# Optimization experiments

Hardware: AMD Instinct MI355X
Metric: run time of the kernel (lower is better)

The kernel has to match this reference:

```python
import jax, jax.numpy as jnp
import numpy as np

B, T, S, H, V, L = 64, 60, 60, 512, 32000, 2
NEG = -1.0e9  # matches torch mask value -1000000000.0


def setup_inputs() -> dict:
    key = jax.random.key(0)
    ks = jax.random.split(key, 12)
    sc = 0.05
    return {
        "indices": jax.random.randint(ks[0], (B, T), 0, V),
        "enc_output": jax.random.normal(ks[1], (B, S, H), dtype=jnp.float32),
        "de_lens": jax.random.randint(ks[2], (B,), 1, S + 1),
        "emb": jax.random.normal(ks[3], (V, H), dtype=jnp.float32) * sc,
        "w_ih": jax.random.normal(ks[4], (L, 4 * H, H), dtype=jnp.float32) * sc,
        "w_hh": jax.random.normal(ks[5], (L, 4 * H, H), dtype=jnp.float32) * sc,
        "b_ih": jnp.zeros((L, 4 * H), dtype=jnp.float32),
        "b_hh": jnp.zeros((L, 4 * H), dtype=jnp.float32),
        "lin_w": jax.random.normal(ks[6], (L, H, 2 * H), dtype=jnp.float32) * sc,
        "lin_b": jnp.zeros((L, H), dtype=jnp.float32),
        "out_w": jax.random.normal(ks[7], (V, H), dtype=jnp.float32) * sc,
        "out_b": jnp.zeros((V,), dtype=jnp.float32),
    }


def _lstm_seq(x, w_ih, w_hh, b_ih, b_hh):
    # x: [B,T,H] -> hidden states [B,T,H]; torch gate order i,f,g,o
    xg = jnp.einsum('bth,gh->btg', x, w_ih) + b_ih  # [B,T,4H]
    h0 = jnp.zeros((x.shape[0], w_hh.shape[1]), x.dtype)

    def step(carry, xg_t):
        h, c = carry
        g = xg_t + h @ w_hh.T + b_hh
        i, f, gg, o = jnp.split(g, 4, axis=-1)
        c = jax.nn.sigmoid(f) * c + jax.nn.sigmoid(i) * jnp.tanh(gg)
        h = jax.nn.sigmoid(o) * jnp.tanh(c)
        return (h, c), h

    _, hs = jax.lax.scan(step, (h0, h0), jnp.swapaxes(xg, 0, 1))
    return jnp.swapaxes(hs, 0, 1)


def reference(indices, enc_output, de_lens, emb, w_ih, w_hh, b_ih, b_hh,
              lin_w, lin_b, out_w, out_b):
    # additive length mask over encoder positions: [B,S]
    mask = jnp.where(jnp.arange(S)[None, :] < de_lens[:, None], 0.0, NEG).astype(enc_output.dtype)
    x = emb[indices]  # [B,T,H]
    for l in range(L):
        dec = _lstm_seq(x, w_ih[l], w_hh[l], b_ih[l], b_hh[l])  # [B,T,H]
        scores = jnp.einsum('bth,bsh->bts', dec, enc_output) + mask[:, None, :]
        probs = jax.nn.softmax(scores, axis=-1)
        attn = jnp.einsum('bts,bsh->bth', probs, enc_output)
        cat = jnp.concatenate([dec, attn], axis=-1)  # [B,T,2H]
        x = jnp.einsum('btk,hk->bth', cat, lin_w[l]) + lin_b[l]
    return jnp.einsum('bth,vh->btv', x, out_w) + out_b  # [B,T,V]
```

## Files before the change

kernel.cpp:

```cpp
#include <hip/hip_runtime.h>
#include <hip/hip_bf16.h>
#include <math.h>

#define B_ 64
#define T_ 60
#define S_ 60
#define H_ 512
#define V_ 32000
#define L_ 2
#define BT_ (B_*T_)
#define LDSROW 40
#define LDSROW2 72

typedef __attribute__((ext_vector_type(8))) short short8;
typedef __attribute__((ext_vector_type(4))) float f32x4;
typedef __attribute__((ext_vector_type(4))) unsigned int u32x4;

__device__ __forceinline__ short f2bf(float x) {
  __hip_bfloat16 h = __float2bfloat16(x);
  return __builtin_bit_cast(short, h);
}
__device__ __forceinline__ float bf2f(short s) {
  unsigned int u = ((unsigned int)(unsigned short)s) << 16;
  return __builtin_bit_cast(float, u);
}
__device__ __forceinline__ float sigm(float x) { return 1.f / (1.f + __expf(-x)); }
__device__ __forceinline__ float tanh_(float x) {
  float e = __expf(-2.f * fabsf(x));
  float t = (1.f - e) / (1.f + e);
  return x >= 0.f ? t : -t;
}

__device__ __forceinline__ void ld4g(const char* p, u32x4* q, bool llc) {
  if (llc)
    asm volatile("global_load_dwordx4 %0, %4, off sc0 sc1\n\t"
                 "global_load_dwordx4 %1, %4, off offset:16 sc0 sc1\n\t"
                 "global_load_dwordx4 %2, %4, off offset:32 sc0 sc1\n\t"
                 "global_load_dwordx4 %3, %4, off offset:48 sc0 sc1"
                 : "=v"(q[0]), "=v"(q[1]), "=v"(q[2]), "=v"(q[3]) : "v"(p));
  else
    asm volatile("global_load_dwordx4 %0, %4, off sc0\n\t"
                 "global_load_dwordx4 %1, %4, off offset:16 sc0\n\t"
                 "global_load_dwordx4 %2, %4, off offset:32 sc0\n\t"
                 "global_load_dwordx4 %3, %4, off offset:48 sc0"
                 : "=v"(q[0]), "=v"(q[1]), "=v"(q[2]), "=v"(q[3]) : "v"(p));
}

#define LDSBAR() do { \
    asm volatile("s_waitcnt lgkmcnt(0)" ::: "memory"); \
    __builtin_amdgcn_s_barrier(); \
    __builtin_amdgcn_sched_barrier(0); \
  } while (0)

__global__ __launch_bounds__(256) void convbf_k(const float* __restrict__ src,
                                                short* __restrict__ dst) {
  int g = blockIdx.x * 256 + threadIdx.x;
  const float* s = src + (size_t)g * 8;
  float4 v0 = *(const float4*)s, v1 = *(const float4*)(s + 4);
  short8 o;
  o[0]=f2bf(v0.x); o[1]=f2bf(v0.y); o[2]=f2bf(v0.z); o[3]=f2bf(v0.w);
  o[4]=f2bf(v1.x); o[5]=f2bf(v1.y); o[6]=f2bf(v1.z); o[7]=f2bf(v1.w);
  *(short8*)(dst + (size_t)g * 8) = o;
}

__global__ __launch_bounds__(256) void pack_whh_k(const float* __restrict__ whh,
                                                  short* __restrict__ pk) {
  int idx = blockIdx.x * 256 + threadIdx.x;
  int l = idx >> 17, rem = idx & 131071;
  int n = rem >> 6, k8 = rem & 63;
  int g = n >> 9, j = n & 511;
  int np = (j >> 4) * 64 + g * 16 + (j & 15);
  const float* src = whh + ((size_t)l * 2048 + n) * 512 + k8 * 8;
  float4 v0 = *(const float4*)src, v1 = *(const float4*)(src + 4);
  short8 o;
  o[0]=f2bf(v0.x); o[1]=f2bf(v0.y); o[2]=f2bf(v0.z); o[3]=f2bf(v0.w);
  o[4]=f2bf(v1.x); o[5]=f2bf(v1.y); o[6]=f2bf(v1.z); o[7]=f2bf(v1.w);
  size_t dst = (size_t)l * (2048 * 512) + ((size_t)((np >> 4) * 64 + k8)) * 128 + (np & 15) * 8;
  *(short8*)(pk + dst) = o;
}

__global__ __launch_bounds__(256) void embed_k(const int* __restrict__ idx,
                                               const float* __restrict__ emb,
                                               float* __restrict__ x) {
  int e = blockIdx.x * 256 + threadIdx.x;
  int bt = e >> 9, h = e & (H_ - 1);
  int row = idx[bt];
  x[e] = emb[(size_t)row * H_ + h];
}

template<bool XPOSE>
__global__ __launch_bounds__(256) void gemm_a32_k(
    const float* __restrict__ A, const float* __restrict__ Bw,
    const float* __restrict__ bias1, const float* __restrict__ bias2,
    float* __restrict__ C, short* __restrict__ Cbf, int M, int N, int K) {
  __shared__ short Ahs[128 * LDSROW];
  __shared__ short Als[128 * LDSROW];
  __shared__ short Bs[128 * LDSROW];
  int tid = threadIdx.x;
  int bm = blockIdx.y * 128, bn = blockIdx.x * 128;
  int wid = tid >> 6, lane = tid & 63;
  int wr = wid >> 1, wc = wid & 1;
  int lrow = lane & 15, lk = (lane >> 4) * 8;
  f32x4 acc[4][4];
#pragma unroll
  for (int i = 0; i < 4; ++i)
#pragma unroll
    for (int j = 0; j < 4; ++j) acc[i][j] = (f32x4){0.f, 0.f, 0.f, 0.f};

  int srow = tid >> 2, scol = (tid & 3) * 8;

  for (int k0 = 0; k0 < K; k0 += 32) {
#pragma unroll
    for (int it = 0; it < 2; ++it) {
      int r = srow + it * 64;
      const float* ap = A + (size_t)(bm + r) * K + k0 + scol;
      float4 a0 = *(const float4*)ap, a1 = *(const float4*)(ap + 4);
      float av[8] = {a0.x,a0.y,a0.z,a0.w,a1.x,a1.y,a1.z,a1.w};
      short8 hv, lv;
#pragma unroll
      for (int e = 0; e < 8; ++e) {
        short h = f2bf(av[e]);
        hv[e] = h;
        lv[e] = f2bf(av[e] - bf2f(h));
      }
      *(short8*)(Ahs + r * LDSROW + scol) = hv;
      *(short8*)(Als + r * LDSROW + scol) = lv;
      const float* bp = Bw + (size_t)(bn + r) * K + k0 + scol;
      float4 b0 = *(const float4*)bp, b1 = *(const float4*)(bp + 4);
      short8 bv;
      bv[0]=f2bf(b0.x); bv[1]=f2bf(b0.y); bv[2]=f2bf(b0.z); bv[3]=f2bf(b0.w);
      bv[4]=f2bf(b1.x); bv[5]=f2bf(b1.y); bv[6]=f2bf(b1.z); bv[7]=f2bf(b1.w);
      *(short8*)(Bs + r * LDSROW + scol) = bv;
    }
    __syncthreads();
    short8 ah[4], al[4], bfr[4];
#pragma unroll
    for (int i = 0; i < 4; ++i) {
      ah[i] = *(const short8*)(Ahs + (wr * 64 + i * 16 + lrow) * LDSROW + lk);
      al[i] = *(const short8*)(Als + (wr * 64 + i * 16 + lrow) * LDSROW + lk);
    }
#pragma unroll
    for (int j = 0; j < 4; ++j)
      bfr[j] = *(const short8*)(Bs + (wc * 64 + j * 16 + lrow) * LDSROW + lk);
#pragma unroll
    for (int i = 0; i < 4; ++i)
#pragma unroll
      for (int j = 0; j < 4; ++j) {
        acc[i][j] = __builtin_amdgcn_mfma_f32_16x16x32_bf16(ah[i], bfr[j], acc[i][j], 0, 0, 0);
        acc[i][j] = __builtin_amdgcn_mfma_f32_16x16x32_bf16(al[i], bfr[j], acc[i][j], 0, 0, 0);
      }
    __syncthreads();
  }

#pragma unroll
  for (int j = 0; j < 4; ++j) {
    int col = bn + wc * 64 + j * 16 + lrow;
    float bv = bias1[col] + (bias2 ? bias2[col] : 0.f);
#pragma unroll
    for (int i = 0; i < 4; ++i) {
#pragma unroll
      for (int r = 0; r < 4; ++r) {
        int row = bm + wr * 64 + i * 16 + (lane >> 4) * 4 + r;
        float v = acc[i][j][r] + bv;
        if (XPOSE) {
          int b = row / T_, t = row - b * T_;
          int g = col >> 9, jg = col & 511;
          int c8 = b >> 3, bloc = b & 7, q = jg >> 6;
          int nploc = ((jg >> 4) & 3) * 64 + g * 16 + (jg & 15);
          C[(((size_t)t * 64 + q * 8 + c8) * 8 + bloc) * 256 + nploc] = v;
        } else {
          C[(size_t)row * N + col] = v;
          if (Cbf) Cbf[(size_t)row * N + col] = f2bf(v);
        }
      }
    }
  }
}

__global__ __launch_bounds__(256) void gemm_bb_k(
    const short* __restrict__ A, const short* __restrict__ Bbf,
    const float* __restrict__ bias, float* __restrict__ C) {
  const int N = V_, K = H_;
  int n = blockIdx.x;
  int xcd = n & 7, pos = n >> 3;
  int base = (xcd < 4) ? xcd * 938 : 4 * 938 + (xcd - 4) * 937;
  int wg = base + pos;
  int bm = (wg % 30) * 128;
  int bn = (wg / 30) * 128;

  __shared__ short As[128 * LDSROW2];
  __shared__ short Bs[128 * LDSROW2];
  int tid = threadIdx.x;
  int wid = tid >> 6, lane = tid & 63;
  int wr = wid >> 1, wc = wid & 1;
  int lrow = lane & 15;
  f32x4 acc[4][4];
#pragma unroll
  for (int i = 0; i < 4; ++i)
#pragma unroll
    for (int j = 0; j < 4; ++j) acc[i][j] = (f32x4){0.f, 0.f, 0.f, 0.f};

  int srow = tid >> 2, scol = (tid & 3) * 16;

  for (int k0 = 0; k0 < K; k0 += 64) {
#pragma unroll
    for (int it = 0; it < 2; ++it) {
      int r = srow + it * 64;
      const short* ap = A + (size_t)(bm + r) * K + k0 + scol;
      short8 a0 = *(const short8*)ap, a1 = *(const short8*)(ap + 8);
      *(short8*)(As + r * LDSROW2 + scol) = a0;
      *(short8*)(As + r * LDSROW2 + scol + 8) = a1;
      const short* bp = Bbf + (size_t)(bn + r) * K + k0 + scol;
      short8 b0 = *(const short8*)bp, b1 = *(const short8*)(bp + 8);
      *(short8*)(Bs + r * LDSROW2 + scol) = b0;
      *(short8*)(Bs + r * LDSROW2 + scol + 8) = b1;
    }
    __syncthreads();
#pragma unroll
    for (int kk = 0; kk < 2; ++kk) {
      int lk = kk * 32 + (lane >> 4) * 8;
      short8 af[4], bfr[4];
#pragma unroll
      for (int i = 0; i < 4; ++i)
        af[i] = *(const short8*)(As + (wr * 64 + i * 16 + lrow) * LDSROW2 + lk);
#pragma unroll
      for (int j = 0; j < 4; ++j)
        bfr[j] = *(const short8*)(Bs + (wc * 64 + j * 16 + lrow) * LDSROW2 + lk);
#pragma unroll
      for (int i = 0; i < 4; ++i)
#pragma unroll
        for (int j = 0; j < 4; ++j)
          acc[i][j] = __builtin_amdgcn_mfma_f32_16x16x32_bf16(af[i], bfr[j], acc[i][j], 0, 0, 0);
    }
    __syncthreads();
  }

#pragma unroll
  for (int j = 0; j < 4; ++j) {
    int col = bn + wc * 64 + j * 16 + lrow;
    float bv = bias[col];
#pragma unroll
    for (int i = 0; i < 4; ++i)
#pragma unroll
      for (int r = 0; r < 4; ++r) {
        int row = bm + wr * 64 + i * 16 + (lane >> 4) * 4 + r;
        float v = acc[i][j][r] + bv;
        float* cp = C + (size_t)row * N + col;
        asm volatile("global_store_dword %0, %1, off nt" :: "v"(cp), "v"(v) : "memory");
      }
  }
}

__global__ __launch_bounds__(512, 2) void lstm_seq_k(
    const float* __restrict__ xg,
    const short* __restrict__ whh_pk,
    char* __restrict__ hx,
    float* __restrict__ dec) {
  __shared__ short hhi[16][520];
  __shared__ short hlo[16][520];
  __shared__ float gates[256][20];
  const int tid = threadIdx.x;
  const int bid = blockIdx.x;
  const int c = bid & 7, q = bid >> 3;
  const int w = tid >> 6, lane = tid & 63;
  const int lr = lane & 15, lkg = lane >> 4;

  for (int i = tid; i < 16 * 520; i += 512) {
    ((short*)hhi)[i] = 0;
    ((short*)hlo)[i] = 0;
  }

  short8 wreg[2][16];
#pragma unroll
  for (int nt = 0; nt < 2; ++nt)
#pragma unroll
    for (int kt = 0; kt < 16; ++kt)
      wreg[nt][kt] = *(const short8*)(whh_pk +
          ((size_t)((q * 16 + w * 2 + nt) * 64 + kt * 4 + lkg)) * 128 + lr * 8);

  const bool epi = (tid < 256);
  const int bloc_e = tid & 7;
  const int p_e = (tid >> 3) & 31;
  const int j0 = p_e * 2;
  const int s = tid & 255;
  char* grp = hx + (size_t)c * 65536;

  float cc0 = 0.f, cc1 = 0.f;
  __syncthreads();

  for (int t = 0; t < T_; ++t) {
    const unsigned tgt = (unsigned)t;
    float2 xgv[4];
    const int rw0 = (j0 >> 4) * 64 + (j0 & 15);
    if (epi) {
      const float* xb = xg + ((size_t)t * 64 + bid) * 2048 + bloc_e * 256;
#pragma unroll
      for (int g = 0; g < 4; ++g) xgv[g] = *(const float2*)(xb + rw0 + g * 16);
      asm volatile("" ::: "memory");
    } else {
      const char* base = grp + (size_t)(t & 1) * 32768;
      const char* pA = base + (size_t)s * 64;
      const char* pB = base + (size_t)(s + 256) * 64;
      u32x4 qA[4], qB[4];
      ld4g(pA, qA, false);
      ld4g(pB, qB, false);
      for (unsigned a = 0;; ++a) {
        asm volatile("s_waitcnt vmcnt(0)" ::: "memory");
        __builtin_amdgcn_sched_barrier(0);
        unsigned bad = 0;
#pragma unroll
        for (int i = 0; i < 4; ++i) bad |= (qA[i][2] ^ tgt) | (qB[i][2] ^ tgt);
        if (!bad) break;
        __builtin_amdgcn_s_sleep(1);
        bool llc = (a & 1) != 0;
        ld4g(pA, qA, llc);
        ld4g(pB, qB, llc);
      }
      u32x4 hA = {qA[0][0], qA[1][0], qA[2][0], qA[3][0]};
      u32x4 lA = {qA[0][1], qA[1][1], qA[2][1], qA[3][1]};
      u32x4 hB = {qB[0][0], qB[1][0], qB[2][0], qB[3][0]};
      u32x4 lB = {qB[0][1], qB[1][1], qB[2][1], qB[3][1]};
      *(u32x4*)(&hhi[s >> 6][(s & 63) * 8]) = hA;
      *(u32x4*)(&hlo[s >> 6][(s & 63) * 8]) = lA;
      *(u32x4*)(&hhi[4 + (s >> 6)][(s & 63) * 8]) = hB;
      *(u32x4*)(&hlo[4 + (s >> 6)][(s & 63) * 8]) = lB;
    }
    LDSBAR();

    f32x4 acc[2];
    acc[0] = (f32x4){0.f, 0.f, 0.f, 0.f};
    acc[1] = (f32x4){0.f, 0.f, 0.f, 0.f};
#pragma unroll
    for (int kt = 0; kt < 16; ++kt) {
      short8 ah = *(const short8*)(&hhi[lr][kt * 32 + lkg * 8]);
      short8 al = *(const short8*)(&hlo[lr][kt * 32 + lkg * 8]);
#pragma unroll
      for (int nt = 0; nt < 2; ++nt) {
        acc[nt] = __builtin_amdgcn_mfma_f32_16x16x32_bf16(ah, wreg[nt][kt], acc[nt], 0, 0, 0);
        acc[nt] = __builtin_amdgcn_mfma_f32_16x16x32_bf16(al, wreg[nt][kt], acc[nt], 0, 0, 0);
      }
    }
#pragma unroll
    for (int nt = 0; nt < 2; ++nt)
      *(f32x4*)(&gates[(w * 2 + nt) * 16 + lr][lkg * 4]) = acc[nt];
    LDSBAR();

    if (epi) {
      float gv0[4], gv1[4];
#pragma unroll
      for (int g = 0; g < 4; ++g) {
        int rw = rw0 + g * 16;
        gv0[g] = gates[rw][bloc_e] + xgv[g].x;
        gv1[g] = gates[rw + 1][bloc_e] + xgv[g].y;
      }
      float cn0 = sigm(gv0[1]) * cc0 + sigm(gv0[0]) * tanh_(gv0[2]);
      float hn0 = sigm(gv0[3]) * tanh_(cn0);
      cc0 = cn0;
      float cn1 = sigm(gv1[1]) * cc1 + sigm(gv1[0]) * tanh_(gv1[2]);
      float hn1 = sigm(gv1[3]) * tanh_(cn1);
      cc1 = cn1;
      short hi0 = f2bf(hn0), hi1 = f2bf(hn1);
      short lo0 = f2bf(hn0 - bf2f(hi0)), lo1 = f2bf(hn1 - bf2f(hi1));
      u32x4 hv;
      hv[0] = (unsigned)(unsigned short)hi0 | ((unsigned)(unsigned short)hi1 << 16);
      hv[1] = (unsigned)(unsigned short)lo0 | ((unsigned)(unsigned short)lo1 << 16);
      hv[2] = tgt + 1u;
      hv[3] = tgt + 1u;
      char* pb = grp + (size_t)((t + 1) & 1) * 32768 +
                 ((size_t)(bloc_e * 256 + q * 32 + p_e)) * 16;
      asm volatile("global_store_dwordx4 %0, %1, off sc0" :: "v"(pb), "v"(hv) : "memory");
      asm volatile("global_store_dwordx4 %0, %1, off sc0 sc1" :: "v"(pb), "v"(hv) : "memory");
      float2 dv; dv.x = hn0; dv.y = hn1;
      *(float2*)(dec + ((size_t)(c * 8 + bloc_e) * T_ + t) * H_ + q * 64 + j0) = dv;
    }
    LDSBAR();
  }
}

__global__ __launch_bounds__(256) void attn_k(const float* __restrict__ dec,
                                              const float* __restrict__ enc,
                                              const int* __restrict__ lens,
                                              float* __restrict__ cat) {
  int bt = blockIdx.x;
  int b = bt / T_;
  __shared__ float dsh[H_];
  __shared__ float p[64];
  int tid = threadIdx.x;
  dsh[tid] = dec[(size_t)bt * H_ + tid];
  dsh[tid + 256] = dec[(size_t)bt * H_ + tid + 256];
  __syncthreads();
  int wid = tid >> 6, lane = tid & 63;
  int len = lens[b];
  for (int s = wid; s < S_; s += 4) {
    const float* er = enc + ((size_t)(b * S_ + s)) * H_ + lane * 8;
    float4 e0 = *(const float4*)er, e1 = *(const float4*)(er + 4);
    const float* dr = dsh + lane * 8;
    float sum = e0.x*dr[0] + e0.y*dr[1] + e0.z*dr[2] + e0.w*dr[3]
              + e1.x*dr[4] + e1.y*dr[5] + e1.z*dr[6] + e1.w*dr[7];
#pragma unroll
    for (int off = 32; off > 0; off >>= 1) sum += __shfl_down(sum, off);
    if (lane == 0) p[s] = sum + (s < len ? 0.f : -1.0e9f);
  }
  __syncthreads();
  if (wid == 0) {
    float v = (lane < S_) ? p[lane] : -INFINITY;
    float m = v;
#pragma unroll
    for (int off = 32; off > 0; off >>= 1) m = fmaxf(m, __shfl_down(m, off));
    m = __shfl(m, 0);
    float e = (lane < S_) ? expf(v - m) : 0.f;
    float ssum = e;
#pragma unroll
    for (int off = 32; off > 0; off >>= 1) ssum += __shfl_down(ssum, off);
    ssum = __shfl(ssum, 0);
    if (lane < S_) p[lane] = e / ssum;
  }
  __syncthreads();
  int h = tid * 2;
  float a0 = 0.f, a1 = 0.f;
  for (int s = 0; s < S_; ++s) {
    float ps = p[s];
    const float* er = enc + ((size_t)(b * S_ + s)) * H_ + h;
    a0 += ps * er[0];
    a1 += ps * er[1];
  }
  size_t base = (size_t)bt * (2 * H_);
  cat[base + h]          = dsh[h];
  cat[base + h + 1]      = dsh[h + 1];
  cat[base + H_ + h]     = a0;
  cat[base + H_ + h + 1] = a1;
}

extern "C" void kernel_launch(void* const* d_in, const int* in_sizes, int n_in,
                              void* d_out, int out_size, void* d_ws, size_t ws_size,
                              hipStream_t stream) {
  (void)in_sizes; (void)n_in; (void)out_size; (void)ws_size;
  const int*   indices = (const int*)d_in[0];
  const float* enc     = (const float*)d_in[1];
  const int*   de_lens = (const int*)d_in[2];
  const float* emb     = (const float*)d_in[3];
  const float* w_ih    = (const float*)d_in[4];
  const float* w_hh    = (const float*)d_in[5];
  const float* b_ih    = (const float*)d_in[6];
  const float* b_hh    = (const float*)d_in[7];
  const float* lin_w   = (const float*)d_in[8];
  const float* lin_b   = (const float*)d_in[9];
  const float* out_w   = (const float*)d_in[10];
  const float* out_b   = (const float*)d_in[11];
  float* outp = (float*)d_out;

  char* ws = (char*)d_ws;
  size_t off = 0;
  auto alloc = [&](size_t bytes) -> void* {
    void* p = ws + off; off += (bytes + 255) & ~(size_t)255; return p;
  };
  float* x      = (float*)alloc((size_t)BT_ * H_ * 4);
  float* xg     = (float*)alloc((size_t)BT_ * 4 * H_ * 4);
  float* dec    = (float*)alloc((size_t)BT_ * H_ * 4);
  float* cat    = (float*)alloc((size_t)BT_ * 2 * H_ * 4);
  short* ow_bf  = (short*)alloc((size_t)V_ * H_ * 2);
  short* whh_pk = (short*)alloc((size_t)L_ * 4 * H_ * H_ * 2);
  short* x_bf   = (short*)alloc((size_t)BT_ * H_ * 2);
  char*  hx     = (char*)alloc((size_t)8 * 2 * 32768);

  convbf_k<<<V_ * H_ / 8 / 256, 256, 0, stream>>>(out_w, ow_bf);
  pack_whh_k<<<L_ * 2048 * 64 / 256, 256, 0, stream>>>(w_hh, whh_pk);
  embed_k<<<BT_ * H_ / 256, 256, 0, stream>>>(indices, emb, x);

  for (int l = 0; l < L_; ++l) {
    gemm_a32_k<true><<<dim3(4 * H_ / 128, BT_ / 128), 256, 0, stream>>>(
        x, w_ih + (size_t)l * 4 * H_ * H_, b_ih + l * 4 * H_, b_hh + l * 4 * H_,
        xg, nullptr, BT_, 4 * H_, H_);
    hipMemsetAsync(hx, 0, (size_t)8 * 2 * 32768, stream);
    lstm_seq_k<<<64, 512, 0, stream>>>(
        xg, whh_pk + (size_t)l * 4 * H_ * H_, hx, dec);
    attn_k<<<BT_, 256, 0, stream>>>(dec, enc, de_lens, cat);
    gemm_a32_k<false><<<dim3(H_ / 128, BT_ / 128), 256, 0, stream>>>(
        cat, lin_w + (size_t)l * H_ * 2 * H_, lin_b + l * H_, nullptr,
        x, (l == L_ - 1) ? x_bf : nullptr, BT_, H_, 2 * H_);
  }

  gemm_bb_k<<<30 * (V_ / 128), 256, 0, stream>>>(x_bf, ow_bf, out_b, outp);
}
```

Baseline: 980.0 us.

## Precompute bf16 hi/lo activation splits and bf16 weights for LSTM input and linear GEMMs

Producers (embedding, attention, linear GEMM epilogue) now write activations as bf16 hi/lo pairs instead of fp32, and w_ih/lin_w are converted to bf16 once up front. The GEMM loads pre-split bf16 tiles directly with a K-step of 64 and no per-tile conversion. This cuts global read bytes and in-loop conversion ALU in the GEMMs. In exchange it adds two weight conversion kernels and extra conversion work in the producers.

```diff
diff --git a/kernel.cpp b/kernel.cpp
--- a/kernel.cpp
+++ b/kernel.cpp
@@ -9,7 +9,6 @@
 #define V_ 32000
 #define L_ 2
 #define BT_ (B_*T_)
-#define LDSROW 40
 #define LDSROW2 72
 
 typedef __attribute__((ext_vector_type(8))) short short8;
@@ -81,74 +80,71 @@
 
 __global__ __launch_bounds__(256) void embed_k(const int* __restrict__ idx,
                                                const float* __restrict__ emb,
-                                               float* __restrict__ x) {
+                                               short* __restrict__ xhi,
+                                               short* __restrict__ xlo) {
   int e = blockIdx.x * 256 + threadIdx.x;
   int bt = e >> 9, h = e & (H_ - 1);
   int row = idx[bt];
-  x[e] = emb[(size_t)row * H_ + h];
+  float v = emb[(size_t)row * H_ + h];
+  short hi = f2bf(v);
+  xhi[e] = hi;
+  xlo[e] = f2bf(v - bf2f(hi));
 }
 
 template<bool XPOSE>
-__global__ __launch_bounds__(256) void gemm_a32_k(
-    const float* __restrict__ A, const float* __restrict__ Bw,
+__global__ __launch_bounds__(256) void gemm_hl_k(
+    const short* __restrict__ Ahi, const short* __restrict__ Alo,
+    const short* __restrict__ Bbf,
     const float* __restrict__ bias1, const float* __restrict__ bias2,
-    float* __restrict__ C, short* __restrict__ Cbf, int M, int N, int K) {
-  __shared__ short Ahs[128 * LDSROW];
-  __shared__ short Als[128 * LDSROW];
-  __shared__ short Bs[128 * LDSROW];
+    float* __restrict__ C, short* __restrict__ Chi, short* __restrict__ Clo,
+    int M, int N, int K) {
+  __shared__ short Ahs[128 * LDSROW2];
+  __shared__ short Als[128 * LDSROW2];
+  __shared__ short Bs[128 * LDSROW2];
   int tid = threadIdx.x;
   int bm = blockIdx.y * 128, bn = blockIdx.x * 128;
   int wid = tid >> 6, lane = tid & 63;
   int wr = wid >> 1, wc = wid & 1;
-  int lrow = lane & 15, lk = (lane >> 4) * 8;
+  int lrow = lane & 15;
   f32x4 acc[4][4];
 #pragma unroll
   for (int i = 0; i < 4; ++i)
 #pragma unroll
     for (int j = 0; j < 4; ++j) acc[i][j] = (f32x4){0.f, 0.f, 0.f, 0.f};
 
-  int srow = tid >> 2, scol = (tid & 3) * 8;
-
-  for (int k0 = 0; k0 < K; k0 += 32) {
-#pragma unroll
-    for (int it = 0; it < 2; ++it) {
-      int r = srow + it * 64;
-      const float* ap = A + (size_t)(bm + r) * K + k0 + scol;
-      float4 a0 = *(const float4*)ap, a1 = *(const float4*)(ap + 4);
-      float av[8] = {a0.x,a0.y,a0.z,a0.w,a1.x,a1.y,a1.z,a1.w};
-      short8 hv, lv;
-#pragma unroll
-      for (int e = 0; e < 8; ++e) {
-        short h = f2bf(av[e]);
-        hv[e] = h;
-        lv[e] = f2bf(av[e] - bf2f(h));
-      }
-      *(short8*)(Ahs + r * LDSROW + scol) = hv;
-      *(short8*)(Als + r * LDSROW + scol) = lv;
-      const float* bp = Bw + (size_t)(bn + r) * K + k0 + scol;
-      float4 b0 = *(const float4*)bp, b1 = *(const float4*)(bp + 4);
-      short8 bv;
-      bv[0]=f2bf(b0.x); bv[1]=f2bf(b0.y); bv[2]=f2bf(b0.z); bv[3]=f2bf(b0.w);
-      bv[4]=f2bf(b1.x); bv[5]=f2bf(b1.y); bv[6]=f2bf(b1.z); bv[7]=f2bf(b1.w);
-      *(short8*)(Bs + r * LDSROW + scol) = bv;
+  int srow = tid >> 1, scol = (tid & 1) * 32;
+
+  for (int k0 = 0; k0 < K; k0 += 64) {
+    const short* ahp = Ahi + (size_t)(bm + srow) * K + k0 + scol;
+    const short* alp = Alo + (size_t)(bm + srow) * K + k0 + scol;
+    const short* bp  = Bbf + (size_t)(bn + srow) * K + k0 + scol;
+#pragma unroll
+    for (int u = 0; u < 4; ++u) {
+      *(short8*)(Ahs + srow * LDSROW2 + scol + u * 8) = *(const short8*)(ahp + u * 8);
+      *(short8*)(Als + srow * LDSROW2 + scol + u * 8) = *(const short8*)(alp + u * 8);
+      *(short8*)(Bs  + srow * LDSROW2 + scol + u * 8) = *(const short8*)(bp  + u * 8);
     }
     __syncthreads();
-    short8 ah[4], al[4], bfr[4];
-#pragma unroll
-    for (int i = 0; i < 4; ++i) {
-      ah[i] = *(const short8*)(Ahs + (wr * 64 + i * 16 + lrow) * LDSROW + lk);
-      al[i] = *(const short8*)(Als + (wr * 64 + i * 16 + lrow) * LDSROW + lk);
-    }
-#pragma unroll
-    for (int j = 0; j < 4; ++j)
-      bfr[j] = *(const short8*)(Bs + (wc * 64 + j * 16 + lrow) * LDSROW + lk);
-#pragma unroll
-    for (int i = 0; i < 4; ++i)
-#pragma unroll
-      for (int j = 0; j < 4; ++j) {
-        acc[i][j] = __builtin_amdgcn_mfma_f32_16x16x32_bf16(ah[i], bfr[j], acc[i][j], 0, 0, 0);
-        acc[i][j] = __builtin_amdgcn_mfma_f32_16x16x32_bf16(al[i], bfr[j], acc[i][j], 0, 0, 0);
-      }
+#pragma unroll
+    for (int kk = 0; kk < 2; ++kk) {
+      int lk = kk * 32 + (lane >> 4) * 8;
+      short8 ah[4], al[4], bfr[4];
+#pragma unroll
+      for (int i = 0; i < 4; ++i) {
+        ah[i] = *(const short8*)(Ahs + (wr * 64 + i * 16 + lrow) * LDSROW2 + lk);
+        al[i] = *(const short8*)(Als + (wr * 64 + i * 16 + lrow) * LDSROW2 + lk);
+      }
+#pragma unroll
+      for (int j = 0; j < 4; ++j)
+        bfr[j] = *(const short8*)(Bs + (wc * 64 + j * 16 + lrow) * LDSROW2 + lk);
+#pragma unroll
+      for (int i = 0; i < 4; ++i)
+#pragma unroll
+        for (int j = 0; j < 4; ++j) {
+          acc[i][j] = __builtin_amdgcn_mfma_f32_16x16x32_bf16(ah[i], bfr[j], acc[i][j], 0, 0, 0);
+          acc[i][j] = __builtin_amdgcn_mfma_f32_16x16x32_bf16(al[i], bfr[j], acc[i][j], 0, 0, 0);
+        }
+    }
     __syncthreads();
   }
 
@@ -169,8 +165,9 @@
           int nploc = ((jg >> 4) & 3) * 64 + g * 16 + (jg & 15);
           C[(((size_t)t * 64 + q * 8 + c8) * 8 + bloc) * 256 + nploc] = v;
         } else {
-          C[(size_t)row * N + col] = v;
-          if (Cbf) Cbf[(size_t)row * N + col] = f2bf(v);
+          short hi = f2bf(v);
+          Chi[(size_t)row * N + col] = hi;
+          Clo[(size_t)row * N + col] = f2bf(v - bf2f(hi));
         }
       }
     }
@@ -380,7 +377,8 @@
 __global__ __launch_bounds__(256) void attn_k(const float* __restrict__ dec,
                                               const float* __restrict__ enc,
                                               const int* __restrict__ lens,
-                                              float* __restrict__ cat) {
+                                              short* __restrict__ cat_hi,
+                                              short* __restrict__ cat_lo) {
   int bt = blockIdx.x;
   int b = bt / T_;
   __shared__ float dsh[H_];
@@ -425,10 +423,14 @@
     a1 += ps * er[1];
   }
   size_t base = (size_t)bt * (2 * H_);
-  cat[base + h]          = dsh[h];
-  cat[base + h + 1]      = dsh[h + 1];
-  cat[base + H_ + h]     = a0;
-  cat[base + H_ + h + 1] = a1;
+  float vv[4] = {dsh[h], dsh[h + 1], a0, a1};
+  int   oo[4] = {h, h + 1, H_ + h, H_ + h + 1};
+#pragma unroll
+  for (int i = 0; i < 4; ++i) {
+    short hi = f2bf(vv[i]);
+    cat_hi[base + oo[i]] = hi;
+    cat_lo[base + oo[i]] = f2bf(vv[i] - bf2f(hi));
+  }
 }
 
 extern "C" void kernel_launch(void* const* d_in, const int* in_sizes, int n_in,
@@ -454,31 +456,38 @@
   auto alloc = [&](size_t bytes) -> void* {
     void* p = ws + off; off += (bytes + 255) & ~(size_t)255; return p;
   };
-  float* x      = (float*)alloc((size_t)BT_ * H_ * 4);
+  short* x_hi   = (short*)alloc((size_t)BT_ * H_ * 2);
+  short* x_lo   = (short*)alloc((size_t)BT_ * H_ * 2);
   float* xg     = (float*)alloc((size_t)BT_ * 4 * H_ * 4);
   float* dec    = (float*)alloc((size_t)BT_ * H_ * 4);
-  float* cat    = (float*)alloc((size_t)BT_ * 2 * H_ * 4);
+  short* cat_hi = (short*)alloc((size_t)BT_ * 2 * H_ * 2);
+  short* cat_lo = (short*)alloc((size_t)BT_ * 2 * H_ * 2);
   short* ow_bf  = (short*)alloc((size_t)V_ * H_ * 2);
+  short* wih_bf = (short*)alloc((size_t)L_ * 4 * H_ * H_ * 2);
+  short* linw_bf= (short*)alloc((size_t)L_ * H_ * 2 * H_ * 2);
   short* whh_pk = (short*)alloc((size_t)L_ * 4 * H_ * H_ * 2);
-  short* x_bf   = (short*)alloc((size_t)BT_ * H_ * 2);
   char*  hx     = (char*)alloc((size_t)8 * 2 * 32768);
 
   convbf_k<<<V_ * H_ / 8 / 256, 256, 0, stream>>>(out_w, ow_bf);
+  convbf_k<<<L_ * 4 * H_ * H_ / 8 / 256, 256, 0, stream>>>(w_ih, wih_bf);
+  convbf_k<<<L_ * H_ * 2 * H_ / 8 / 256, 256, 0, stream>>>(lin_w, linw_bf);
   pack_whh_k<<<L_ * 2048 * 64 / 256, 256, 0, stream>>>(w_hh, whh_pk);
-  embed_k<<<BT_ * H_ / 256, 256, 0, stream>>>(indices, emb, x);
+  embed_k<<<BT_ * H_ / 256, 256, 0, stream>>>(indices, emb, x_hi, x_lo);
 
   for (int l = 0; l < L_; ++l) {
-    gemm_a32_k<true><<<dim3(4 * H_ / 128, BT_ / 128), 256, 0, stream>>>(
-        x, w_ih + (size_t)l * 4 * H_ * H_, b_ih + l * 4 * H_, b_hh + l * 4 * H_,
-        xg, nullptr, BT_, 4 * H_, H_);
+    gemm_hl_k<true><<<dim3(4 * H_ / 128, BT_ / 128), 256, 0, stream>>>(
+        x_hi, x_lo, wih_bf + (size_t)l * 4 * H_ * H_,
+        b_ih + l * 4 * H_, b_hh + l * 4 * H_,
+        xg, nullptr, nullptr, BT_, 4 * H_, H_);
     hipMemsetAsync(hx, 0, (size_t)8 * 2 * 32768, stream);
     lstm_seq_k<<<64, 512, 0, stream>>>(
         xg, whh_pk + (size_t)l * 4 * H_ * H_, hx, dec);
-    attn_k<<<BT_, 256, 0, stream>>>(dec, enc, de_lens, cat);
-    gemm_a32_k<false><<<dim3(H_ / 128, BT_ / 128), 256, 0, stream>>>(
-        cat, lin_w + (size_t)l * H_ * 2 * H_, lin_b + l * H_, nullptr,
-        x, (l == L_ - 1) ? x_bf : nullptr, BT_, H_, 2 * H_);
-  }
-
-  gemm_bb_k<<<30 * (V_ / 128), 256, 0, stream>>>(x_bf, ow_bf, out_b, outp);
-}
+    attn_k<<<BT_, 256, 0, stream>>>(dec, enc, de_lens, cat_hi, cat_lo);
+    gemm_hl_k<false><<<dim3(H_ / 128, BT_ / 128), 256, 0, stream>>>(
+        cat_hi, cat_lo, linw_bf + (size_t)l * H_ * 2 * H_,
+        lin_b + l * H_, nullptr,
+        nullptr, x_hi, x_lo, BT_, H_, 2 * H_);
+  }
+
+  gemm_bb_k<<<30 * (V_ / 128), 256, 0, stream>>>(x_hi, ow_bf, out_b, outp);
+}
```

After: 956.0 us. 2.4% less time.
